# Kernel optimization log

Hardware: AMD Instinct MI355X
Metric: run time of the kernel (lower is better)

## Reference

```python
import jax, jax.numpy as jnp
import numpy as np

EPS_COS = 1e-8
EPS_SHARP = 1e-16


def setup_inputs() -> dict:
    key = jax.random.key(0)
    k1, k2, k3, k4 = jax.random.split(key, 4)
    B, H, R, C, M = 512, 512, 2048, 64, 3
    out_dim = 3 * C + 2 * M + 4  # 202
    h = jax.random.normal(k1, (B, H), dtype=jnp.float32)
    prev_w = jax.random.uniform(k2, (B, R), dtype=jnp.float32)
    prev_w = prev_w / prev_w.sum(axis=1, keepdims=True)  # valid focus distribution
    memory = jax.random.normal(k3, (B, R, C), dtype=jnp.float32)
    fc_w = jax.random.normal(k4, (out_dim, H), dtype=jnp.float32) * 0.05
    fc_b = jnp.zeros((out_dim,), dtype=jnp.float32)
    return {"h": h, "prev_w": prev_w, "memory": memory, "fc_w": fc_w, "fc_b": fc_b}


def _write_head(h, prev_w, memory, fc_w, fc_b):
    B, R, C = memory.shape
    total = fc_w.shape[0]
    shift_len = total - 3 * C - 3          # 2*max_shift + 1
    m = (shift_len - 1) // 2               # max_shift

    z = h @ fc_w.T + fc_b                  # [B, total]
    sizes = [C, 1, 1, shift_len, 1, C, C]
    offs = np.cumsum([0] + sizes)
    k     = jnp.tanh(z[:, offs[0]:offs[1]])                 # [B, C]
    beta  = jax.nn.softplus(z[:, offs[1]:offs[2]])          # [B, 1]
    g     = jax.nn.sigmoid(z[:, offs[2]:offs[3]])           # [B, 1]
    s     = jax.nn.softmax(z[:, offs[3]:offs[4]], axis=1)   # [B, 2m+1]
    gamma = jax.nn.softplus(z[:, offs[4]:offs[5]]) + 1.0    # [B, 1]
    e     = jax.nn.sigmoid(z[:, offs[5]:offs[6]])           # [B, C]
    a     = jnp.tanh(z[:, offs[6]:offs[7]])                 # [B, C]

    # content addressing: cosine similarity of k vs each memory row
    num = jnp.einsum('bc,brc->br', k, memory)
    k_n = jnp.maximum(jnp.linalg.norm(k, axis=1, keepdims=True), EPS_COS)   # [B,1]
    m_n = jnp.maximum(jnp.linalg.norm(memory, axis=2), EPS_COS)             # [B,R]
    w_c = jax.nn.softmax(beta * (num / (k_n * m_n)), axis=1)                # [B,R]

    # gated interpolation
    w_g = g * w_c + (1.0 - g) * prev_w                                      # [B,R]

    # circular shift (per-sample cross-correlation, O(B*R*(2m+1)))
    unrolled = jnp.concatenate([w_g[:, -m:], w_g, w_g[:, :m]], axis=1)      # [B, R+2m]
    windows = jnp.stack([unrolled[:, j:j + R] for j in range(2 * m + 1)], axis=1)  # [B,2m+1,R]
    w_s = jnp.einsum('bjr,bj->br', windows, s)                              # [B,R]

    # sharpen
    w_p = jnp.power(w_s, gamma)
    w = w_p / (w_p.sum(axis=1, keepdims=True) + EPS_SHARP)                  # [B,R]

    # erase + write (fused)
    wE = w[:, :, None]                                                      # [B,R,1]
    new_mem = memory * (1.0 - wE * e[:, None, :]) + wE * a[:, None, :]      # [B,R,C]
    return w, new_mem


def reference(h, prev_w, memory, fc_w, fc_b):
    return _write_head(h, prev_w, memory, fc_w, fc_b)
```

## Files before the change

### kernel.cpp

```cpp
#include <hip/hip_runtime.h>
#include <math.h>

#define BB 512
#define HH 512
#define RR 2048
#define CC 64
#define OUTD 202
#define PSTRIDE 208
#define K_OFF 0
#define E_OFF 64
#define A_OFF 128
#define S_OFF 192
#define COMBO_OFF 199
#define G_OFF 200
#define GAMMA_OFF 201

#define PART_STRIDE 224

typedef float f32x4 __attribute__((ext_vector_type(4)));

__device__ __forceinline__ float softplusf_(float x) {
    return (x > 20.f) ? x : log1pf(expf(x));
}
__device__ __forceinline__ float sigmoidf_(float x) {
    return 1.f / (1.f + expf(-x));
}

__global__ __launch_bounds__(256) void params_part_kernel(
    const float* __restrict__ h, const float* __restrict__ fc_w,
    float* __restrict__ part)
{
    __shared__ float h_sh[8][128];
    const int tid = threadIdx.x;
    const int bg = blockIdx.x >> 2;
    const int hq = blockIdx.x & 3;
    const int b0 = bg * 8;
    const int h0 = hq * 128;

    for (int idx = tid; idx < 8 * 128; idx += 256) {
        int j = idx >> 7, i = idx & 127;
        h_sh[j][i] = h[(size_t)(b0 + j) * HH + h0 + i];
    }
    __syncthreads();

    if (tid < OUTD) {
        float acc[8];
        #pragma unroll
        for (int j = 0; j < 8; ++j) acc[j] = 0.f;
        const float4* wr = (const float4*)(fc_w + (size_t)tid * HH + h0);
        #pragma unroll 4
        for (int i4 = 0; i4 < 32; ++i4) {
            float4 wv = wr[i4];
            int i = i4 * 4;
            #pragma unroll
            for (int j = 0; j < 8; ++j) {
                acc[j] = fmaf(wv.x, h_sh[j][i + 0], acc[j]);
                acc[j] = fmaf(wv.y, h_sh[j][i + 1], acc[j]);
                acc[j] = fmaf(wv.z, h_sh[j][i + 2], acc[j]);
                acc[j] = fmaf(wv.w, h_sh[j][i + 3], acc[j]);
            }
        }
        #pragma unroll
        for (int j = 0; j < 8; ++j) {
            part[((size_t)(b0 + j) * 4 + hq) * PART_STRIDE + tid] = acc[j];
        }
    }
}

__global__ __launch_bounds__(256) void params_combine_kernel(
    const float* __restrict__ part, const float* __restrict__ fc_b,
    float* __restrict__ pw)
{
    __shared__ float z_sh[80];
    const int b = blockIdx.x;
    const int tid = threadIdx.x;
    float* p = pw + (size_t)b * PSTRIDE;

    if (tid < OUTD) {
        const float* q = part + (size_t)b * 4 * PART_STRIDE + tid;
        float z = q[0] + q[PART_STRIDE] + q[2 * PART_STRIDE]
                + q[3 * PART_STRIDE] + fc_b[tid];
        if (tid < 74) z_sh[tid] = z;
        if (tid < 64)                      p[K_OFF + tid] = tanhf(z);
        else if (tid == 65)                p[G_OFF] = sigmoidf_(z);
        else if (tid == 73)                p[GAMMA_OFF] = softplusf_(z) + 1.f;
        else if (tid >= 74 && tid < 138)   p[E_OFF + (tid - 74)] = sigmoidf_(z);
        else if (tid >= 138)               p[A_OFF + (tid - 138)] = tanhf(z);
    }
    __syncthreads();

    if (tid < 64) {
        float kv = tanhf(z_sh[tid]);
        float ss = kv * kv;
        #pragma unroll
        for (int m = 1; m < 64; m <<= 1) ss += __shfl_xor(ss, m, 64);
        if (tid == 0) {
            float kn = fmaxf(sqrtf(ss), 1e-8f);
            float beta = softplusf_(z_sh[64]);
            p[COMBO_OFF] = beta / kn;
            float mx = -1e30f;
            #pragma unroll
            for (int q = 0; q < 7; ++q) mx = fmaxf(mx, z_sh[66 + q]);
            float ev[7], se = 0.f;
            #pragma unroll
            for (int q = 0; q < 7; ++q) {
                ev[q] = __expf(z_sh[66 + q] - mx);
                se += ev[q];
            }
            float inv = 1.f / se;
            #pragma unroll
            for (int q = 0; q < 7; ++q) p[S_OFF + q] = ev[q] * inv;
        }
    }
}

__device__ __forceinline__ float block_reduce_sum4(float v, float* red) {
    #pragma unroll
    for (int m = 1; m < 64; m <<= 1) v += __shfl_xor(v, m, 64);
    int wid = threadIdx.x >> 6;
    if ((threadIdx.x & 63) == 0) red[wid] = v;
    __syncthreads();
    float x = red[0] + red[1] + red[2] + red[3];
    __syncthreads();
    return x;
}

__global__ __launch_bounds__(256) void score_kernel(
    const float* __restrict__ memory, const float* __restrict__ pw,
    float* __restrict__ sc, float* __restrict__ esum)
{
    __shared__ float red[4];
    const int tid = threadIdx.x;
    const int b = blockIdx.x >> 2;
    const int rbase = (blockIdx.x & 3) * 512;
    const int lane16 = tid & 15;
    const int rgrp = tid >> 4;
    const float* p = pw + (size_t)b * PSTRIDE;
    const float4 k4 = *(const float4*)(p + K_OFF + lane16 * 4);
    const float combo = p[COMBO_OFF];
    const float* memb = memory + (size_t)b * RR * CC;

    float lsum = 0.f;
    #pragma unroll
    for (int mi = 0; mi < 4; ++mi) {
        float4 m4[8];
        #pragma unroll
        for (int j = 0; j < 8; ++j) {
            int r = rbase + (mi * 8 + j) * 16 + rgrp;
            m4[j] = *(const float4*)(memb + (size_t)r * CC + lane16 * 4);
        }
        #pragma unroll
        for (int j = 0; j < 8; ++j) {
            int r = rbase + (mi * 8 + j) * 16 + rgrp;
            float num = m4[j].x * k4.x + m4[j].y * k4.y + m4[j].z * k4.z
                      + m4[j].w * k4.w;
            float ssq = m4[j].x * m4[j].x + m4[j].y * m4[j].y
                      + m4[j].z * m4[j].z + m4[j].w * m4[j].w;
            #pragma unroll
            for (int m = 1; m < 16; m <<= 1) {
                num += __shfl_xor(num, m, 64);
                ssq += __shfl_xor(ssq, m, 64);
            }
            if (lane16 == 0) {
                float mn = fmaxf(sqrtf(ssq), 1e-8f);
                float ev = __expf(combo * num / mn);
                sc[(size_t)b * RR + r] = ev;
                lsum += ev;
            }
        }
    }
    float bs = block_reduce_sum4(lsum, red);
    if (tid == 0) esum[blockIdx.x] = bs;
}

__global__ __launch_bounds__(256) void weight_kernel(
    const float* __restrict__ sc, const float* __restrict__ esum,
    const float* __restrict__ prev_w, const float* __restrict__ pw,
    float* __restrict__ out_w)
{
    __shared__ float buf[RR];
    __shared__ float wg[RR];
    __shared__ float red[4];
    const int b = blockIdx.x;
    const int tid = threadIdx.x;
    const float* p = pw + (size_t)b * PSTRIDE;
    const float g = p[G_OFF];
    const float gamma = p[GAMMA_OFF];
    const float s0 = p[S_OFF + 0], s1 = p[S_OFF + 1], s2 = p[S_OFF + 2],
                s3 = p[S_OFF + 3], s4 = p[S_OFF + 4], s5 = p[S_OFF + 5],
                s6 = p[S_OFF + 6];
    const float* eb = esum + (size_t)b * 4;
    const float se = eb[0] + eb[1] + eb[2] + eb[3];
    const float gi = g / se, omg = 1.f - g;

    #pragma unroll
    for (int t = 0; t < 4; ++t) {
        int r2 = (t * 256 + tid) * 2;
        float2 ev = *(const float2*)(sc + (size_t)b * RR + r2);
        float2 pv = *(const float2*)(prev_w + (size_t)b * RR + r2);
        wg[r2]     = gi * ev.x + omg * pv.x;
        wg[r2 + 1] = gi * ev.y + omg * pv.y;
    }
    __syncthreads();

    float lp = 0.f;
    #pragma unroll
    for (int t = 0; t < 8; ++t) {
        int r = t * 256 + tid;
        float acc = s0 * wg[(r - 3) & (RR - 1)]
                  + s1 * wg[(r - 2) & (RR - 1)]
                  + s2 * wg[(r - 1) & (RR - 1)]
                  + s3 * wg[r]
                  + s4 * wg[(r + 1) & (RR - 1)]
                  + s5 * wg[(r + 2) & (RR - 1)]
                  + s6 * wg[(r + 3) & (RR - 1)];
        float v = __powf(acc, gamma);
        buf[r] = v;
        lp += v;
    }
    const float ps = block_reduce_sum4(lp, red);
    const float invp = 1.f / (ps + 1e-16f);

    #pragma unroll
    for (int t = 0; t < 4; ++t) {
        int r2 = (t * 256 + tid) * 2;
        *(float2*)(out_w + (size_t)b * RR + r2) =
            make_float2(buf[r2] * invp, buf[r2 + 1] * invp);
    }
}

__global__ __launch_bounds__(256) void update_kernel(
    const float* __restrict__ memory, const float* __restrict__ w,
    const float* __restrict__ pw, float* __restrict__ out_mem)
{
    const int bid = (int)gridDim.x - 1 - (int)blockIdx.x;
    const int b = bid >> 2;
    const int rbase = (bid & 3) * 512;
    const int tid = threadIdx.x;
    const int lane8 = tid & 7;
    const int rgrp = tid >> 3;
    const float* p = pw + (size_t)b * PSTRIDE;
    const f32x4 ea = *(const f32x4*)(p + E_OFF + lane8 * 8);
    const f32x4 eb2 = *(const f32x4*)(p + E_OFF + lane8 * 8 + 4);
    const f32x4 aa = *(const f32x4*)(p + A_OFF + lane8 * 8);
    const f32x4 ab = *(const f32x4*)(p + A_OFF + lane8 * 8 + 4);
    const float* memb = memory + (size_t)b * RR * CC;
    float* omb = out_mem + (size_t)b * RR * CC;
    const float* wb = w + (size_t)b * RR;

    #pragma unroll
    for (int mi = 0; mi < 2; ++mi) {
        f32x4 ma[8], mb[8];
        float wv[8];
        #pragma unroll
        for (int j = 0; j < 8; ++j) {
            int r = rbase + (mi * 8 + j) * 32 + rgrp;
            const f32x4* mp = (const f32x4*)(memb + (size_t)r * CC + lane8 * 8);
            ma[j] = mp[0];
            mb[j] = mp[1];
            wv[j] = wb[r];
        }
        #pragma unroll
        for (int j = 0; j < 8; ++j) {
            int r = rbase + (mi * 8 + j) * 32 + rgrp;
            f32x4 oa, ob;
            oa.x = ma[j].x * (1.f - wv[j] * ea.x) + wv[j] * aa.x;
            oa.y = ma[j].y * (1.f - wv[j] * ea.y) + wv[j] * aa.y;
            oa.z = ma[j].z * (1.f - wv[j] * ea.z) + wv[j] * aa.z;
            oa.w = ma[j].w * (1.f - wv[j] * ea.w) + wv[j] * aa.w;
            ob.x = mb[j].x * (1.f - wv[j] * eb2.x) + wv[j] * ab.x;
            ob.y = mb[j].y * (1.f - wv[j] * eb2.y) + wv[j] * ab.y;
            ob.z = mb[j].z * (1.f - wv[j] * eb2.z) + wv[j] * ab.z;
            ob.w = mb[j].w * (1.f - wv[j] * eb2.w) + wv[j] * ab.w;
            f32x4* op = (f32x4*)(omb + (size_t)r * CC + lane8 * 8);
            op[0] = oa;
            op[1] = ob;
        }
    }
}

extern "C" void kernel_launch(void* const* d_in, const int* in_sizes, int n_in,
                              void* d_out, int out_size, void* d_ws, size_t ws_size,
                              hipStream_t stream) {
    const float* h      = (const float*)d_in[0];
    const float* prev_w = (const float*)d_in[1];
    const float* memory = (const float*)d_in[2];
    const float* fc_w   = (const float*)d_in[3];
    const float* fc_b   = (const float*)d_in[4];

    float* pw      = (float*)d_ws;
    float* out_w   = (float*)d_out;
    float* out_mem = out_w + (size_t)BB * RR;

    const size_t pw_f   = (size_t)BB * PSTRIDE;
    const size_t br_f   = (size_t)BB * RR;
    const size_t es_f   = (size_t)BB * 4;
    const size_t part_f = (size_t)BB * 4 * PART_STRIDE;
    const size_t need_f = pw_f + br_f + es_f + part_f;

    float* sc   = pw + pw_f;
    float* esum = sc + br_f;
    float* part = esum + es_f;

    if (ws_size >= need_f * sizeof(float)) {
        params_part_kernel<<<256, 256, 0, stream>>>(h, fc_w, part);
        params_combine_kernel<<<BB, 256, 0, stream>>>(part, fc_b, pw);
        score_kernel<<<BB * 4, 256, 0, stream>>>(memory, pw, sc, esum);
        weight_kernel<<<BB, 256, 0, stream>>>(sc, esum, prev_w, pw, out_w);
        update_kernel<<<BB * 4, 256, 0, stream>>>(memory, out_w, pw, out_mem);
    } else {
        float* sc_fb   = out_mem;
        float* esum_fb = pw + pw_f;
        float* part_fb = esum_fb + es_f;
        params_part_kernel<<<256, 256, 0, stream>>>(h, fc_w, part_fb);
        params_combine_kernel<<<BB, 256, 0, stream>>>(part_fb, fc_b, pw);
        score_kernel<<<BB * 4, 256, 0, stream>>>(memory, pw, sc_fb, esum_fb);
        weight_kernel<<<BB, 256, 0, stream>>>(sc_fb, esum_fb, prev_w, pw, out_w);
        update_kernel<<<BB * 4, 256, 0, stream>>>(memory, out_w, pw, out_mem);
    }
}
```

Before: 189.6 us.

## Fuse weight computation into memory update kernel with redundant per-chunk recompute

```diff
diff --git a/kernel.cpp b/kernel.cpp
--- a/kernel.cpp
+++ b/kernel.cpp
@@ -173,6 +173,99 @@
     if (tid == 0) esum[blockIdx.x] = bs;
 }
 
+__global__ __launch_bounds__(256) void wupdate_kernel(
+    const float* __restrict__ memory, const float* __restrict__ sc,
+    const float* __restrict__ esum, const float* __restrict__ prev_w,
+    const float* __restrict__ pw, float* __restrict__ out_w,
+    float* __restrict__ out_mem)
+{
+    __shared__ float wgs[RR + 6];
+    __shared__ float wps[RR];
+    __shared__ float red[4];
+
+    const int bid = (int)gridDim.x - 1 - (int)blockIdx.x;
+    const int b = bid >> 2;
+    const int rbase = (bid & 3) * 512;
+    const int tid = threadIdx.x;
+    const float* p = pw + (size_t)b * PSTRIDE;
+    const float g = p[G_OFF];
+    const float gamma = p[GAMMA_OFF];
+    const float s0 = p[S_OFF + 0], s1 = p[S_OFF + 1], s2 = p[S_OFF + 2],
+                s3 = p[S_OFF + 3], s4 = p[S_OFF + 4], s5 = p[S_OFF + 5],
+                s6 = p[S_OFF + 6];
+    const float* eb = esum + (size_t)b * 4;
+    const float se = eb[0] + eb[1] + eb[2] + eb[3];
+    const float gi = g / se, omg = 1.f - g;
+
+    const float* scb = sc + (size_t)b * RR;
+    const float* pvb = prev_w + (size_t)b * RR;
+    for (int idx = tid; idx < RR + 6; idx += 256) {
+        int r = (idx - 3) & (RR - 1);
+        wgs[idx] = gi * scb[r] + omg * pvb[r];
+    }
+    __syncthreads();
+
+    float lp = 0.f;
+    #pragma unroll
+    for (int t = 0; t < 8; ++t) {
+        int r = t * 256 + tid;
+        float acc = s0 * wgs[r]     + s1 * wgs[r + 1]
+                  + s2 * wgs[r + 2] + s3 * wgs[r + 3]
+                  + s4 * wgs[r + 4] + s5 * wgs[r + 5]
+                  + s6 * wgs[r + 6];
+        float v = __powf(acc, gamma);
+        wps[r] = v;
+        lp += v;
+    }
+    const float ps = block_reduce_sum4(lp, red);
+    const float invp = 1.f / (ps + 1e-16f);
+
+    {
+        int r2 = rbase + tid * 2;
+        *(float2*)(out_w + (size_t)b * RR + r2) =
+            make_float2(wps[r2] * invp, wps[r2 + 1] * invp);
+    }
+
+    const int lane8 = tid & 7;
+    const int rgrp = tid >> 3;
+    const f32x4 ea = *(const f32x4*)(p + E_OFF + lane8 * 8);
+    const f32x4 eb2 = *(const f32x4*)(p + E_OFF + lane8 * 8 + 4);
+    const f32x4 aa = *(const f32x4*)(p + A_OFF + lane8 * 8);
+    const f32x4 ab = *(const f32x4*)(p + A_OFF + lane8 * 8 + 4);
+    const float* memb = memory + (size_t)b * RR * CC;
+    float* omb = out_mem + (size_t)b * RR * CC;
+
+    #pragma unroll
+    for (int mi = 0; mi < 4; ++mi) {
+        f32x4 ma[4], mb[4];
+        float wv[4];
+        #pragma unroll
+        for (int j = 0; j < 4; ++j) {
+            int r = rbase + (mi * 4 + j) * 32 + rgrp;
+            const f32x4* mp = (const f32x4*)(memb + (size_t)r * CC + lane8 * 8);
+            ma[j] = mp[0];
+            mb[j] = mp[1];
+            wv[j] = wps[r] * invp;
+        }
+        #pragma unroll
+        for (int j = 0; j < 4; ++j) {
+            int r = rbase + (mi * 4 + j) * 32 + rgrp;
+            f32x4 oa, ob;
+            oa.x = ma[j].x * (1.f - wv[j] * ea.x) + wv[j] * aa.x;
+            oa.y = ma[j].y * (1.f - wv[j] * ea.y) + wv[j] * aa.y;
+            oa.z = ma[j].z * (1.f - wv[j] * ea.z) + wv[j] * aa.z;
+            oa.w = ma[j].w * (1.f - wv[j] * ea.w) + wv[j] * aa.w;
+            ob.x = mb[j].x * (1.f - wv[j] * eb2.x) + wv[j] * ab.x;
+            ob.y = mb[j].y * (1.f - wv[j] * eb2.y) + wv[j] * ab.y;
+            ob.z = mb[j].z * (1.f - wv[j] * eb2.z) + wv[j] * ab.z;
+            ob.w = mb[j].w * (1.f - wv[j] * eb2.w) + wv[j] * ab.w;
+            f32x4* op = (f32x4*)(omb + (size_t)r * CC + lane8 * 8);
+            op[0] = oa;
+            op[1] = ob;
+        }
+    }
+}
+
 __global__ __launch_bounds__(256) void weight_kernel(
     const float* __restrict__ sc, const float* __restrict__ esum,
     const float* __restrict__ prev_w, const float* __restrict__ pw,
@@ -249,20 +342,20 @@
     const float* wb = w + (size_t)b * RR;
 
     #pragma unroll
-    for (int mi = 0; mi < 2; ++mi) {
-        f32x4 ma[8], mb[8];
-        float wv[8];
-        #pragma unroll
-        for (int j = 0; j < 8; ++j) {
-            int r = rbase + (mi * 8 + j) * 32 + rgrp;
+    for (int mi = 0; mi < 4; ++mi) {
+        f32x4 ma[4], mb[4];
+        float wv[4];
+        #pragma unroll
+        for (int j = 0; j < 4; ++j) {
+            int r = rbase + (mi * 4 + j) * 32 + rgrp;
             const f32x4* mp = (const f32x4*)(memb + (size_t)r * CC + lane8 * 8);
             ma[j] = mp[0];
             mb[j] = mp[1];
             wv[j] = wb[r];
         }
         #pragma unroll
-        for (int j = 0; j < 8; ++j) {
-            int r = rbase + (mi * 8 + j) * 32 + rgrp;
+        for (int j = 0; j < 4; ++j) {
+            int r = rbase + (mi * 4 + j) * 32 + rgrp;
             f32x4 oa, ob;
             oa.x = ma[j].x * (1.f - wv[j] * ea.x) + wv[j] * aa.x;
             oa.y = ma[j].y * (1.f - wv[j] * ea.y) + wv[j] * aa.y;
@@ -306,8 +399,8 @@
         params_part_kernel<<<256, 256, 0, stream>>>(h, fc_w, part);
         params_combine_kernel<<<BB, 256, 0, stream>>>(part, fc_b, pw);
         score_kernel<<<BB * 4, 256, 0, stream>>>(memory, pw, sc, esum);
-        weight_kernel<<<BB, 256, 0, stream>>>(sc, esum, prev_w, pw, out_w);
-        update_kernel<<<BB * 4, 256, 0, stream>>>(memory, out_w, pw, out_mem);
+        wupdate_kernel<<<BB * 4, 256, 0, stream>>>(memory, sc, esum, prev_w,
+                                                   pw, out_w, out_mem);
     } else {
         float* sc_fb   = out_mem;
         float* esum_fb = pw + pw_f;
```

Result: no change. 189.8 us (+0.1%).
